# Kernel tuning notes

Hardware: AMD Instinct MI355X
Metric: run time of the kernel (lower is better)

## Reference

```python
import jax, jax.numpy as jnp
import numpy as np

LAYER = 2
B, L, N, N2, S, M, D = 128, 50, 12, 12, 20, 12, 100


def _l2norm(x, eps=1e-12):
    # torch F.normalize: x / max(||x||_2, eps) over last dim
    n = jnp.sqrt(jnp.sum(x * x, axis=-1, keepdims=True))
    return x / jnp.maximum(n, eps)


def setup_inputs() -> dict:
    key = jax.random.key(0)
    ks = jax.random.split(key, 10)
    return {
        "sess_self": jax.random.normal(ks[0], (B, L, D), jnp.float32),
        "sess_neighbor": jax.random.normal(ks[1], (B, L, N, D), jnp.float32),
        "sess_neighbor2": jax.random.normal(ks[2], (B, L, N, N2, D), jnp.float32),
        "tar_self": jax.random.normal(ks[3], (B, S, D), jnp.float32),
        "tar_neighbor": jax.random.normal(ks[4], (B, S, M, D), jnp.float32),
        "w1": jax.random.normal(ks[5], (LAYER, D, D), jnp.float32) * 0.1,
        "w2": jax.random.normal(ks[6], (LAYER, D, 1), jnp.float32) * 0.1,
        "w3": jax.random.normal(ks[7], (LAYER, 2 * D, D), jnp.float32) * 0.1,
        "w4": jax.random.normal(ks[8], (LAYER, D, 1), jnp.float32) * 0.1,
        "session_len": jax.random.randint(ks[9], (B,), 1, 50).astype(jnp.int64),
    }


def _forward(sess_self, sess_neighbor, sess_neighbor2, tar_self, tar_neighbor, w1, w2, w3, w4):
    b, s = sess_self.shape[0], tar_self.shape[1]
    l, d = sess_self.shape[1], sess_self.shape[2]
    # sess_embedding_layer: list of [B,S,L,D]; target: list of [B,S,D]
    sess_layers = [jnp.broadcast_to(sess_self[:, None, :, :], (b, s, l, d))]
    tar_layers = [tar_self]
    sn = sess_neighbor  # may be updated by 2-hop aggregation
    for i in range(LAYER):
        # --- session neighbor attention: mul -> linear -> leaky_relu -> linear -> softmax(N) -> sum ---
        mean_sess = jnp.mean(sess_layers[i], axis=1)                     # [B,L,D]
        att = (mean_sess[:, :, None, :] * sn) @ w1[i]                    # [B,L,N,D]
        att = jax.nn.leaky_relu(att, negative_slope=0.2)
        att = jax.nn.softmax(att @ w2[i], axis=-2)                       # [B,L,N,1]
        total = jnp.sum(att * sn, axis=-2)                               # [B,L,D]
        emb = _l2norm(total)
        sess_layers.append(jnp.broadcast_to(emb[:, None, :, :], (b, s, l, d)))
        # --- 2-hop neighbor aggregation (only first layer when layer>1) ---
        if i <= 0 and LAYER > 1:
            att2 = (sn[:, :, :, None, :] * sess_neighbor2) @ w1[i]       # [B,L,N,N2,D]
            att2 = jax.nn.leaky_relu(att2, negative_slope=0.2)
            att2 = jax.nn.softmax(att2 @ w2[i], axis=-2)                 # [B,L,N,N2,1]
            sn = jnp.sum(att2 * sess_neighbor2, axis=-2)                 # [B,L,N,D]
        # --- target neighbor attention ---
        sess_last = sess_layers[i - 1][:, :, :1, :]                      # [B,S,1,D]
        t = tar_layers[i]                                                # [B,S,D]
        cat = jnp.concatenate(
            [t[:, :, None, :] * tar_neighbor, sess_last + tar_neighbor], axis=-1)  # [B,S,M,2D]
        a = jnp.tanh(cat @ w3[i])                                        # [B,S,M,D]
        a = jax.nn.softmax(a @ w4[i], axis=-2)                           # [B,S,M,1]
        tot = jnp.sum(a * tar_neighbor, axis=-2)                         # [B,S,D]
        ti = _l2norm((tot + tar_layers[0]) * 0.5)
        tar_layers.append(ti)
        tar_layers = tar_layers + tar_layers  # faithful: list doubles each layer
    return jnp.stack(sess_layers, axis=0), jnp.stack(tar_layers, axis=0)


def reference(sess_self, sess_neighbor, sess_neighbor2, tar_self, tar_neighbor, w1, w2, w3, w4, session_len):
    return _forward(sess_self, sess_neighbor, sess_neighbor2, tar_self, tar_neighbor, w1, w2, w3, w4)
```

## Files before the change

kernel.cpp:

```cpp
#include <hip/hip_runtime.h>
#include <cmath>

#define CB 128
#define CL 50
#define CN 12
#define CS 20
#define CM 12
#define CD 100

typedef __attribute__((ext_vector_type(8))) short short8;
typedef __attribute__((ext_vector_type(4))) float f32x4;

__device__ __forceinline__ unsigned short f2bf(float f) {
    unsigned int u = __float_as_uint(f);
    u += 0x7FFFu + ((u >> 16) & 1u);
    return (unsigned short)(u >> 16);
}
__device__ __forceinline__ float4 mul4(float4 a, float4 b) {
    return make_float4(a.x * b.x, a.y * b.y, a.z * b.z, a.w * b.w);
}
__device__ __forceinline__ float4 add4(float4 a, float4 b) {
    return make_float4(a.x + b.x, a.y + b.y, a.z + b.z, a.w + b.w);
}
__device__ __forceinline__ short8 pack8(float4 a, float4 b) {
    short8 v;
    v[0] = (short)f2bf(a.x); v[1] = (short)f2bf(a.y);
    v[2] = (short)f2bf(a.z); v[3] = (short)f2bf(a.w);
    v[4] = (short)f2bf(b.x); v[5] = (short)f2bf(b.y);
    v[6] = (short)f2bf(b.z); v[7] = (short)f2bf(b.w);
    return v;
}

__global__ void prep_weights_kernel(const float* __restrict__ w1,
                                    const float* __restrict__ w3,
                                    unsigned short* __restrict__ w1t,
                                    unsigned short* __restrict__ w3t)
{
    int idx = blockIdx.x * 256 + threadIdx.x;
    const int TOT1 = 2 * 112 * 128;
    const int TOT3 = 2 * 112 * 224;
    if (idx < TOT1) {
        int l = idx / (112 * 128);
        int r = idx - l * (112 * 128);
        int n = r / 128, k = r - (r / 128) * 128;
        float v = (n < CD && k < CD) ? w1[l * CD * CD + k * CD + n] : 0.f;
        w1t[idx] = f2bf(v);
    } else if (idx < TOT1 + TOT3) {
        int j = idx - TOT1;
        int l = j / (112 * 224);
        int r = j - l * (112 * 224);
        int n = r / 224, k = r - (r / 224) * 224;
        float v = (n < CD && k < 2 * CD) ? w3[l * 2 * CD * CD + k * CD + n] : 0.f;
        w3t[j] = f2bf(v);
    }
}

__global__ __launch_bounds__(256) void neigh_mfma_kernel(
    const float* __restrict__ a0, const float* __restrict__ c0,
    float* __restrict__ o0, int nb0, int l20,
    const float* __restrict__ a1, const float* __restrict__ c1,
    float* __restrict__ o1, int l21,
    const unsigned short* __restrict__ w1t,
    const float* __restrict__ w2)
{
    __shared__ __align__(16) unsigned short sB[112 * 128];

    const int tid = threadIdx.x;
    const int wave = tid >> 6, lane = tid & 63;
    const int lhi = lane >> 4, llo = lane & 15;

    const float *ap, *cp; float* op; int l2f, g0;
    if ((int)blockIdx.x < nb0) {
        ap = a0; cp = c0; op = o0; l2f = l20; g0 = blockIdx.x * 4;
    } else {
        ap = a1; cp = c1; op = o1; l2f = l21; g0 = (blockIdx.x - nb0) * 4;
    }
    const int g = g0 + wave;

    for (int i = tid; i < 1792; i += 256) {
        int n = i >> 4, kc = i & 15;
        short8 v = *(const short8*)(w1t + n * 128 + kc * 8);
        char* dst = (char*)sB + n * 256 + ((kc ^ (n & 7)) << 4);
        *(short8*)dst = v;
    }

    short8 af[4];
    {
        const int n = (llo < CN) ? llo : 0;
        const float* cpr = cp + ((size_t)g * CN + n) * CD;
        const float* apr = ap + (size_t)g * CD;
#pragma unroll
        for (int ks = 0; ks < 4; ++ks) {
            const int k0 = ks * 32 + lhi * 8;
            if (ks < 3) {
                float4 cv0 = *(const float4*)(cpr + k0);
                float4 cv1 = *(const float4*)(cpr + k0 + 4);
                float4 av0 = *(const float4*)(apr + k0);
                float4 av1 = *(const float4*)(apr + k0 + 4);
                af[ks] = pack8(mul4(av0, cv0), mul4(av1, cv1));
            } else if (lhi == 0) {
                float4 cv0 = *(const float4*)(cpr + 96);
                float4 av0 = *(const float4*)(apr + 96);
                float4 z = make_float4(0.f, 0.f, 0.f, 0.f);
                af[ks] = pack8(mul4(av0, cv0), z);
            } else {
                af[ks] = (short8){0, 0, 0, 0, 0, 0, 0, 0};
            }
        }
    }
    __syncthreads();

    f32x4 acc[7];
#pragma unroll
    for (int nt = 0; nt < 7; ++nt) acc[nt] = (f32x4){0.f, 0.f, 0.f, 0.f};

    const char* pB = (const char*)sB;
    const int bxor = llo & 7;
#pragma unroll
    for (int ks = 0; ks < 4; ++ks) {
        const int kbq = ks * 4 + lhi;
#pragma unroll
        for (int nt = 0; nt < 7; ++nt) {
            short8 bfv = *(const short8*)(pB + (nt * 16 + llo) * 256 + ((kbq ^ bxor) << 4));
            acc[nt] = __builtin_amdgcn_mfma_f32_16x16x32_bf16(af[ks], bfv, acc[nt], 0, 0, 0);
        }
    }

    float s[4] = {0.f, 0.f, 0.f, 0.f};
#pragma unroll
    for (int nt = 0; nt < 7; ++nt) {
        const int n = nt * 16 + llo;
        const float w2v = (n < CD) ? w2[n] : 0.f;
#pragma unroll
        for (int r = 0; r < 4; ++r) {
            float y = acc[nt][r];
            y = (y >= 0.f) ? y : 0.2f * y;
            s[r] = fmaf(y, w2v, s[r]);
        }
    }
#pragma unroll
    for (int off = 1; off < 16; off <<= 1)
#pragma unroll
        for (int r = 0; r < 4; ++r) s[r] += __shfl_xor(s[r], off, 64);

    float pmax = -1e30f;
    if (lhi < 3) pmax = fmaxf(fmaxf(s[0], s[1]), fmaxf(s[2], s[3]));
    pmax = fmaxf(pmax, __shfl_xor(pmax, 16, 64));
    pmax = fmaxf(pmax, __shfl_xor(pmax, 32, 64));
    float e[4];
#pragma unroll
    for (int r = 0; r < 4; ++r) e[r] = (lhi < 3) ? __expf(s[r] - pmax) : 0.f;
    float ps = e[0] + e[1] + e[2] + e[3];
    ps += __shfl_xor(ps, 16, 64);
    ps += __shfl_xor(ps, 32, 64);
    const float inv = 1.f / ps;
    float att[4];
#pragma unroll
    for (int r = 0; r < 4; ++r) att[r] = e[r] * inv;

    float a12[12];
#pragma unroll
    for (int n = 0; n < 12; ++n)
        a12[n] = __shfl(att[n & 3], (n >> 2) * 16, 64);

    const bool act = lane < 50;
    const int d2 = lane * 2;
    float2 tot = make_float2(0.f, 0.f);
    if (act) {
        const float* crow = cp + (size_t)g * CN * CD + d2;
#pragma unroll
        for (int n = 0; n < CN; ++n) {
            float2 cv = *(const float2*)(crow + n * CD);
            tot.x = fmaf(a12[n], cv.x, tot.x);
            tot.y = fmaf(a12[n], cv.y, tot.y);
        }
    }
    if (l2f) {
        float sq = act ? (tot.x * tot.x + tot.y * tot.y) : 0.f;
#pragma unroll
        for (int off = 32; off > 0; off >>= 1) sq += __shfl_xor(sq, off, 64);
        const float rn = 1.f / fmaxf(sqrtf(sq), 1e-12f);
        tot.x *= rn; tot.y *= rn;
    }
    if (act) *(float2*)(op + (size_t)g * CD + d2) = tot;
}

__device__ __forceinline__ int swzq28(int q, int x) {
    return q ^ ((q < 24) ? x : (x & 3));
}
__device__ __forceinline__ float4 xchunk(const float* __restrict__ tnr,
                                         const float* __restrict__ tv,
                                         const float* __restrict__ slv, int k) {
    if (k < CD)
        return mul4(*(const float4*)(tv + k), *(const float4*)(tnr + k));
    if (k < 2 * CD) {
        int k2 = k - CD;
        return add4(*(const float4*)(slv + k2), *(const float4*)(tnr + k2));
    }
    return make_float4(0.f, 0.f, 0.f, 0.f);
}

__global__ __launch_bounds__(256, 3) void tar_mfma_kernel(
    const float* __restrict__ tvec,
    const float* __restrict__ sl,
    const float* __restrict__ tn,
    const unsigned short* __restrict__ w3t,
    const float* __restrict__ w4,
    const float* __restrict__ tar0,
    float* __restrict__ outp,
    int slStride)
{
    __shared__ __align__(16) unsigned short sB[112 * 224];
    __shared__ float s_score[128];
    __shared__ float s_att[96];
    __shared__ float s_sq[8][25];
    __shared__ float s_rn[8];

    const int tid = threadIdx.x;
    const int g0 = blockIdx.x * 8;
    const int wave = tid >> 6, lane = tid & 63;
    const int lhi = lane >> 4, llo = lane & 15;

    for (int i = tid; i < 3136; i += 256) {
        int n = i / 28, kc = i - (i / 28) * 28;
        short8 v = *(const short8*)(w3t + n * 224 + kc * 8);
        char* dst = (char*)sB + n * 448 + (swzq28(kc, n & 7) << 4);
        *(short8*)dst = v;
    }

    short8 af[2][7];
#pragma unroll
    for (int mt = 0; mt < 2; ++mt) {
        const int g = g0 + wave * 2 + mt;
        const int b = g / CS;
        const int m = (llo < CM) ? llo : 0;
        const float* tnr = tn + ((size_t)g * CM + m) * CD;
        const float* tv = tvec + (size_t)g * CD;
        const float* slv = sl + (size_t)b * slStride;
#pragma unroll
        for (int ks = 0; ks < 7; ++ks) {
            const int k0 = ks * 32 + lhi * 8;
            af[mt][ks] = pack8(xchunk(tnr, tv, slv, k0),
                               xchunk(tnr, tv, slv, k0 + 4));
        }
    }
    __syncthreads();

    f32x4 acc[2][7];
#pragma unroll
    for (int mt = 0; mt < 2; ++mt)
#pragma unroll
        for (int nt = 0; nt < 7; ++nt)
            acc[mt][nt] = (f32x4){0.f, 0.f, 0.f, 0.f};

    const char* pB = (const char*)sB;
    const int bxor = llo & 7;
#pragma unroll
    for (int ks = 0; ks < 7; ++ks) {
        const int kbq = ks * 4 + lhi;
        short8 bf[7];
#pragma unroll
        for (int nt = 0; nt < 7; ++nt)
            bf[nt] = *(const short8*)(pB + (nt * 16 + llo) * 448 + (swzq28(kbq, bxor) << 4));
#pragma unroll
        for (int mt = 0; mt < 2; ++mt)
#pragma unroll
            for (int nt = 0; nt < 7; ++nt)
                acc[mt][nt] = __builtin_amdgcn_mfma_f32_16x16x32_bf16(
                    af[mt][ks], bf[nt], acc[mt][nt], 0, 0, 0);
    }

    float w4v[7];
#pragma unroll
    for (int nt = 0; nt < 7; ++nt) {
        int n = nt * 16 + llo;
        w4v[nt] = (n < CD) ? w4[n] : 0.f;
    }
#pragma unroll
    for (int mt = 0; mt < 2; ++mt) {
        float s[4] = {0.f, 0.f, 0.f, 0.f};
#pragma unroll
        for (int nt = 0; nt < 7; ++nt)
#pragma unroll
            for (int r = 0; r < 4; ++r)
                s[r] = fmaf(tanhf(acc[mt][nt][r]), w4v[nt], s[r]);
#pragma unroll
        for (int off = 1; off < 16; off <<= 1)
#pragma unroll
            for (int r = 0; r < 4; ++r) s[r] += __shfl_xor(s[r], off, 64);
        if (llo == 0) {
            int rowb = wave * 32 + mt * 16 + lhi * 4;
#pragma unroll
            for (int r = 0; r < 4; ++r) s_score[rowb + r] = s[r];
        }
    }
    __syncthreads();

    if (tid < 96) {
        const int g = tid / 12;
        const int m = tid - g * 12;
        const float* sr = s_score + g * 16;
        float mx = -1e30f;
#pragma unroll
        for (int j = 0; j < CM; ++j) mx = fmaxf(mx, sr[j]);
        float sum = 0.f;
#pragma unroll
        for (int j = 0; j < CM; ++j) sum += __expf(sr[j] - mx);
        s_att[tid] = __expf(sr[m] - mx) / sum;
    }
    __syncthreads();

    const bool act = tid < 200;
    int gl = tid / 25, d4 = tid % 25;
    float4 tot = make_float4(0.f, 0.f, 0.f, 0.f);
    if (act) {
        const float* tnr = tn + (size_t)(g0 + gl) * CM * CD + d4 * 4;
#pragma unroll
        for (int m = 0; m < CM; ++m) {
            float4 cv = *(const float4*)(tnr + m * CD);
            float at = s_att[gl * CM + m];
            tot.x = fmaf(at, cv.x, tot.x);
            tot.y = fmaf(at, cv.y, tot.y);
            tot.z = fmaf(at, cv.z, tot.z);
            tot.w = fmaf(at, cv.w, tot.w);
        }
        float4 t0 = *(const float4*)(tar0 + (size_t)(g0 + gl) * CD + d4 * 4);
        tot.x = (tot.x + t0.x) * 0.5f;
        tot.y = (tot.y + t0.y) * 0.5f;
        tot.z = (tot.z + t0.z) * 0.5f;
        tot.w = (tot.w + t0.w) * 0.5f;
        s_sq[gl][d4] = tot.x * tot.x + tot.y * tot.y + tot.z * tot.z + tot.w * tot.w;
    }
    __syncthreads();
    if (tid < 8) {
        float sq = 0.f;
        for (int j = 0; j < 25; ++j) sq += s_sq[tid][j];
        s_rn[tid] = 1.f / fmaxf(sqrtf(sq), 1e-12f);
    }
    __syncthreads();
    if (act) {
        float rn = s_rn[gl];
        tot.x *= rn; tot.y *= rn; tot.z *= rn;
        tot.w *= rn;
        *(float4*)(outp + (size_t)(g0 + gl) * CD + d4 * 4) = tot;
    }
}

__global__ void assemble_kernel(
    const float* __restrict__ sess_self, const float* __restrict__ emb0,
    const float* __restrict__ emb1, const float* __restrict__ tar_self,
    const float* __restrict__ T1, const float* __restrict__ T2,
    float4* __restrict__ out)
{
    const int LD4 = CL * CD / 4;
    const int SLD4 = CS * LD4;
    const int LAY0 = CB * SLD4;
    const int TOT0 = 3 * LAY0;
    const int LAY1 = CB * CS * CD / 4;
    const int TOT = TOT0 + 10 * LAY1;

    for (int i = blockIdx.x * blockDim.x + threadIdx.x; i < TOT;
         i += gridDim.x * blockDim.x) {
        float4 v;
        if (i < TOT0) {
            int layer = i / LAY0;
            int r = i - layer * LAY0;
            int b = r / SLD4;
            int r2 = r - b * SLD4;
            int ld4 = r2 % LD4;
            const float* src = (layer == 0) ? sess_self : (layer == 1) ? emb0 : emb1;
            v = ((const float4*)src)[b * LD4 + ld4];
        } else {
            int j = i - TOT0;
            int layer = j / LAY1;
            int r = j - layer * LAY1;
            int k = layer % 5;
            const float* src = (k == 4) ? T2 : ((k == 1) || (k == 3)) ? T1 : tar_self;
            v = ((const float4*)src)[r];
        }
        out[i] = v;
    }
}

extern "C" void kernel_launch(void* const* d_in, const int* in_sizes, int n_in,
                              void* d_out, int out_size, void* d_ws, size_t ws_size,
                              hipStream_t stream)
{
    const float* sess_self      = (const float*)d_in[0];
    const float* sess_neighbor  = (const float*)d_in[1];
    const float* sess_neighbor2 = (const float*)d_in[2];
    const float* tar_self       = (const float*)d_in[3];
    const float* tar_neighbor   = (const float*)d_in[4];
    const float* w1             = (const float*)d_in[5];
    const float* w2             = (const float*)d_in[6];
    const float* w3             = (const float*)d_in[7];
    const float* w4             = (const float*)d_in[8];
    float* out = (float*)d_out;
    float* ws  = (float*)d_ws;

    float* emb0 = ws;
    float* emb1 = ws + 640000;
    float* sn1  = ws + 1280000;
    float* T1   = ws + 8960000;
    float* T2   = ws + 9216000;
    unsigned short* w1t = (unsigned short*)(ws + 9472000);
    unsigned short* w3t = w1t + 28672;

    prep_weights_kernel<<<308, 256, 0, stream>>>(w1, w3, w1t, w3t);

    neigh_mfma_kernel<<<20800, 256, 0, stream>>>(
        sess_self, sess_neighbor, emb0, 1600, 1,
        sess_neighbor, sess_neighbor2, sn1, 0,
        w1t, w2);
    neigh_mfma_kernel<<<1600, 256, 0, stream>>>(
        emb0, sn1, emb1, 1600, 1,
        emb0, sn1, emb1, 1,
        w1t + 112 * 128, w2 + CD);
    tar_mfma_kernel<<<320, 256, 0, stream>>>(
        tar_self, emb0, tar_neighbor, w3t, w4, tar_self, T1, CL * CD);
    tar_mfma_kernel<<<320, 256, 0, stream>>>(
        T1, sess_self, tar_neighbor, w3t + 112 * 224, w4 + CD, tar_self, T2, CL * CD);

    assemble_kernel<<<2048, 256, 0, stream>>>(
        sess_self, emb0, emb1, tar_self, T1, T2, (float4*)out);
}
```

Measured before the change: 292.9 us.

## Rebalance rows per wave in neighbor and target MFMA kernels; nontemporal output stores

The neighbor attention kernel now has each wave handle two row groups instead of one. Each shared-memory B fragment is reused across two MFMAs, and half as many blocks reload the W1 tile into LDS. The target kernel goes the other way: one group per wave with in-register softmax and norm via shuffles, dropping the shared-memory score buffers and extra block barriers, and it launches twice the blocks without the occupancy hint. The assemble kernel switches to nontemporal stores for the large output write. The trade-offs are higher register pressure in the neighbor kernel and more redundant W3 staging in the target kernel.

```diff
diff --git a/kernel.cpp b/kernel.cpp
--- a/kernel.cpp
+++ b/kernel.cpp
@@ -71,11 +71,10 @@
 
     const float *ap, *cp; float* op; int l2f, g0;
     if ((int)blockIdx.x < nb0) {
-        ap = a0; cp = c0; op = o0; l2f = l20; g0 = blockIdx.x * 4;
+        ap = a0; cp = c0; op = o0; l2f = l20; g0 = blockIdx.x * 8;
     } else {
-        ap = a1; cp = c1; op = o1; l2f = l21; g0 = (blockIdx.x - nb0) * 4;
-    }
-    const int g = g0 + wave;
+        ap = a1; cp = c1; op = o1; l2f = l21; g0 = (blockIdx.x - nb0) * 8;
+    }
 
     for (int i = tid; i < 1792; i += 256) {
         int n = i >> 4, kc = i & 15;
@@ -84,8 +83,10 @@
         *(short8*)dst = v;
     }
 
-    short8 af[4];
-    {
+    short8 af[2][4];
+#pragma unroll
+    for (int mt = 0; mt < 2; ++mt) {
+        const int g = g0 + wave * 2 + mt;
         const int n = (llo < CN) ? llo : 0;
         const float* cpr = cp + ((size_t)g * CN + n) * CD;
         const float* apr = ap + (size_t)g * CD;
@@ -97,22 +98,24 @@
                 float4 cv1 = *(const float4*)(cpr + k0 + 4);
                 float4 av0 = *(const float4*)(apr + k0);
                 float4 av1 = *(const float4*)(apr + k0 + 4);
-                af[ks] = pack8(mul4(av0, cv0), mul4(av1, cv1));
+                af[mt][ks] = pack8(mul4(av0, cv0), mul4(av1, cv1));
             } else if (lhi == 0) {
                 float4 cv0 = *(const float4*)(cpr + 96);
                 float4 av0 = *(const float4*)(apr + 96);
                 float4 z = make_float4(0.f, 0.f, 0.f, 0.f);
-                af[ks] = pack8(mul4(av0, cv0), z);
+                af[mt][ks] = pack8(mul4(av0, cv0), z);
             } else {
-                af[ks] = (short8){0, 0, 0, 0, 0, 0, 0, 0};
+                af[mt][ks] = (short8){0, 0, 0, 0, 0, 0, 0, 0};
             }
         }
     }
     __syncthreads();
 
-    f32x4 acc[7];
-#pragma unroll
-    for (int nt = 0; nt < 7; ++nt) acc[nt] = (f32x4){0.f, 0.f, 0.f, 0.f};
+    f32x4 acc[2][7];
+#pragma unroll
+    for (int mt = 0; mt < 2; ++mt)
+#pragma unroll
+        for (int nt = 0; nt < 7; ++nt) acc[mt][nt] = (f32x4){0.f, 0.f, 0.f, 0.f};
 
     const char* pB = (const char*)sB;
     const int bxor = llo & 7;
@@ -122,67 +125,70 @@
 #pragma unroll
         for (int nt = 0; nt < 7; ++nt) {
             short8 bfv = *(const short8*)(pB + (nt * 16 + llo) * 256 + ((kbq ^ bxor) << 4));
-            acc[nt] = __builtin_amdgcn_mfma_f32_16x16x32_bf16(af[ks], bfv, acc[nt], 0, 0, 0);
-        }
-    }
-
-    float s[4] = {0.f, 0.f, 0.f, 0.f};
-#pragma unroll
-    for (int nt = 0; nt < 7; ++nt) {
-        const int n = nt * 16 + llo;
-        const float w2v = (n < CD) ? w2[n] : 0.f;
-#pragma unroll
-        for (int r = 0; r < 4; ++r) {
-            float y = acc[nt][r];
-            y = (y >= 0.f) ? y : 0.2f * y;
-            s[r] = fmaf(y, w2v, s[r]);
-        }
-    }
-#pragma unroll
-    for (int off = 1; off < 16; off <<= 1)
-#pragma unroll
-        for (int r = 0; r < 4; ++r) s[r] += __shfl_xor(s[r], off, 64);
-
-    float pmax = -1e30f;
-    if (lhi < 3) pmax = fmaxf(fmaxf(s[0], s[1]), fmaxf(s[2], s[3]));
-    pmax = fmaxf(pmax, __shfl_xor(pmax, 16, 64));
-    pmax = fmaxf(pmax, __shfl_xor(pmax, 32, 64));
-    float e[4];
-#pragma unroll
-    for (int r = 0; r < 4; ++r) e[r] = (lhi < 3) ? __expf(s[r] - pmax) : 0.f;
-    float ps = e[0] + e[1] + e[2] + e[3];
-    ps += __shfl_xor(ps, 16, 64);
-    ps += __shfl_xor(ps, 32, 64);
-    const float inv = 1.f / ps;
-    float att[4];
-#pragma unroll
-    for (int r = 0; r < 4; ++r) att[r] = e[r] * inv;
-
-    float a12[12];
-#pragma unroll
-    for (int n = 0; n < 12; ++n)
-        a12[n] = __shfl(att[n & 3], (n >> 2) * 16, 64);
+            acc[0][nt] = __builtin_amdgcn_mfma_f32_16x16x32_bf16(af[0][ks], bfv, acc[0][nt], 0, 0, 0);
+            acc[1][nt] = __builtin_amdgcn_mfma_f32_16x16x32_bf16(af[1][ks], bfv, acc[1][nt], 0, 0, 0);
+        }
+    }
+
+    float att[2][4];
+#pragma unroll
+    for (int mt = 0; mt < 2; ++mt) {
+        float s[4] = {0.f, 0.f, 0.f, 0.f};
+#pragma unroll
+        for (int nt = 0; nt < 7; ++nt) {
+            const int n = nt * 16 + llo;
+            const float w2v = (n < CD) ? w2[n] : 0.f;
+#pragma unroll
+            for (int r = 0; r < 4; ++r) {
+                float y = acc[mt][nt][r];
+                y = (y >= 0.f) ? y : 0.2f * y;
+                s[r] = fmaf(y, w2v, s[r]);
+            }
+        }
+#pragma unroll
+        for (int off = 1; off < 16; off <<= 1)
+#pragma unroll
+            for (int r = 0; r < 4; ++r) s[r] += __shfl_xor(s[r], off, 64);
+        float pmax = -1e30f;
+        if (lhi < 3) pmax = fmaxf(fmaxf(s[0], s[1]), fmaxf(s[2], s[3]));
+        pmax = fmaxf(pmax, __shfl_xor(pmax, 16, 64));
+        pmax = fmaxf(pmax, __shfl_xor(pmax, 32, 64));
+        float e[4];
+#pragma unroll
+        for (int r = 0; r < 4; ++r) e[r] = (lhi < 3) ? __expf(s[r] - pmax) : 0.f;
+        float ps = e[0] + e[1] + e[2] + e[3];
+        ps += __shfl_xor(ps, 16, 64);
+        ps += __shfl_xor(ps, 32, 64);
+        const float inv = 1.f / ps;
+#pragma unroll
+        for (int r = 0; r < 4; ++r) att[mt][r] = e[r] * inv;
+    }
 
     const bool act = lane < 50;
     const int d2 = lane * 2;
-    float2 tot = make_float2(0.f, 0.f);
-    if (act) {
-        const float* crow = cp + (size_t)g * CN * CD + d2;
-#pragma unroll
-        for (int n = 0; n < CN; ++n) {
-            float2 cv = *(const float2*)(crow + n * CD);
-            tot.x = fmaf(a12[n], cv.x, tot.x);
-            tot.y = fmaf(a12[n], cv.y, tot.y);
-        }
-    }
-    if (l2f) {
-        float sq = act ? (tot.x * tot.x + tot.y * tot.y) : 0.f;
-#pragma unroll
-        for (int off = 32; off > 0; off >>= 1) sq += __shfl_xor(sq, off, 64);
-        const float rn = 1.f / fmaxf(sqrtf(sq), 1e-12f);
-        tot.x *= rn; tot.y *= rn;
-    }
-    if (act) *(float2*)(op + (size_t)g * CD + d2) = tot;
+#pragma unroll
+    for (int mt = 0; mt < 2; ++mt) {
+        const int g = g0 + wave * 2 + mt;
+        float2 tot = make_float2(0.f, 0.f);
+        if (act) {
+            const float* crow = cp + (size_t)g * CN * CD + d2;
+#pragma unroll
+            for (int n = 0; n < CN; ++n) {
+                const float at = __shfl(att[mt][n & 3], (n >> 2) * 16, 64);
+                float2 cv = *(const float2*)(crow + n * CD);
+                tot.x = fmaf(at, cv.x, tot.x);
+                tot.y = fmaf(at, cv.y, tot.y);
+            }
+        }
+        if (l2f) {
+            float sq = act ? (tot.x * tot.x + tot.y * tot.y) : 0.f;
+#pragma unroll
+            for (int off = 32; off > 0; off >>= 1) sq += __shfl_xor(sq, off, 64);
+            const float rn = 1.f / fmaxf(sqrtf(sq), 1e-12f);
+            tot.x *= rn; tot.y *= rn;
+        }
+        if (act) *(float2*)(op + (size_t)g * CD + d2) = tot;
+    }
 }
 
 __device__ __forceinline__ int swzq28(int q, int x) {
@@ -200,7 +206,7 @@
     return make_float4(0.f, 0.f, 0.f, 0.f);
 }
 
-__global__ __launch_bounds__(256, 3) void tar_mfma_kernel(
+__global__ __launch_bounds__(256) void tar_mfma_kernel(
     const float* __restrict__ tvec,
     const float* __restrict__ sl,
     const float* __restrict__ tn,
@@ -211,15 +217,12 @@
     int slStride)
 {
     __shared__ __align__(16) unsigned short sB[112 * 224];
-    __shared__ float s_score[128];
-    __shared__ float s_att[96];
-    __shared__ float s_sq[8][25];
-    __shared__ float s_rn[8];
 
     const int tid = threadIdx.x;
-    const int g0 = blockIdx.x * 8;
     const int wave = tid >> 6, lane = tid & 63;
     const int lhi = lane >> 4, llo = lane & 15;
+    const int g = blockIdx.x * 4 + wave;
+    const int b = g / CS;
 
     for (int i = tid; i < 3136; i += 256) {
         int n = i / 28, kc = i - (i / 28) * 28;
@@ -228,11 +231,8 @@
         *(short8*)dst = v;
     }
 
-    short8 af[2][7];
-#pragma unroll
-    for (int mt = 0; mt < 2; ++mt) {
-        const int g = g0 + wave * 2 + mt;
-        const int b = g / CS;
+    short8 af[7];
+    {
         const int m = (llo < CM) ? llo : 0;
         const float* tnr = tn + ((size_t)g * CM + m) * CD;
         const float* tv = tvec + (size_t)g * CD;
@@ -240,109 +240,80 @@
 #pragma unroll
         for (int ks = 0; ks < 7; ++ks) {
             const int k0 = ks * 32 + lhi * 8;
-            af[mt][ks] = pack8(xchunk(tnr, tv, slv, k0),
-                               xchunk(tnr, tv, slv, k0 + 4));
+            af[ks] = pack8(xchunk(tnr, tv, slv, k0),
+                           xchunk(tnr, tv, slv, k0 + 4));
         }
     }
     __syncthreads();
 
-    f32x4 acc[2][7];
-#pragma unroll
-    for (int mt = 0; mt < 2; ++mt)
-#pragma unroll
-        for (int nt = 0; nt < 7; ++nt)
-            acc[mt][nt] = (f32x4){0.f, 0.f, 0.f, 0.f};
+    f32x4 acc[7];
+#pragma unroll
+    for (int nt = 0; nt < 7; ++nt) acc[nt] = (f32x4){0.f, 0.f, 0.f, 0.f};
 
     const char* pB = (const char*)sB;
     const int bxor = llo & 7;
 #pragma unroll
     for (int ks = 0; ks < 7; ++ks) {
         const int kbq = ks * 4 + lhi;
-        short8 bf[7];
-#pragma unroll
-        for (int nt = 0; nt < 7; ++nt)
-            bf[nt] = *(const short8*)(pB + (nt * 16 + llo) * 448 + (swzq28(kbq, bxor) << 4));
-#pragma unroll
-        for (int mt = 0; mt < 2; ++mt)
-#pragma unroll
-            for (int nt = 0; nt < 7; ++nt)
-                acc[mt][nt] = __builtin_amdgcn_mfma_f32_16x16x32_bf16(
-                    af[mt][ks], bf[nt], acc[mt][nt], 0, 0, 0);
-    }
-
-    float w4v[7];
+#pragma unroll
+        for (int nt = 0; nt < 7; ++nt) {
+            short8 bfv = *(const short8*)(pB + (nt * 16 + llo) * 448 + (swzq28(kbq, bxor) << 4));
+            acc[nt] = __builtin_amdgcn_mfma_f32_16x16x32_bf16(af[ks], bfv, acc[nt], 0, 0, 0);
+        }
+    }
+
+    float s[4] = {0.f, 0.f, 0.f, 0.f};
 #pragma unroll
     for (int nt = 0; nt < 7; ++nt) {
-        int n = nt * 16 + llo;
-        w4v[nt] = (n < CD) ? w4[n] : 0.f;
-    }
-#pragma unroll
-    for (int mt = 0; mt < 2; ++mt) {
-        float s[4] = {0.f, 0.f, 0.f, 0.f};
-#pragma unroll
-        for (int nt = 0; nt < 7; ++nt)
-#pragma unroll
-            for (int r = 0; r < 4; ++r)
-                s[r] = fmaf(tanhf(acc[mt][nt][r]), w4v[nt], s[r]);
-#pragma unroll
-        for (int off = 1; off < 16; off <<= 1)
-#pragma unroll
-            for (int r = 0; r < 4; ++r) s[r] += __shfl_xor(s[r], off, 64);
-        if (llo == 0) {
-            int rowb = wave * 32 + mt * 16 + lhi * 4;
-#pragma unroll
-            for (int r = 0; r < 4; ++r) s_score[rowb + r] = s[r];
-        }
-    }
-    __syncthreads();
-
-    if (tid < 96) {
-        const int g = tid / 12;
-        const int m = tid - g * 12;
-        const float* sr = s_score + g * 16;
-        float mx = -1e30f;
-#pragma unroll
-        for (int j = 0; j < CM; ++j) mx = fmaxf(mx, sr[j]);
-        float sum = 0.f;
-#pragma unroll
-        for (int j = 0; j < CM; ++j) sum += __expf(sr[j] - mx);
-        s_att[tid] = __expf(sr[m] - mx) / sum;
-    }
-    __syncthreads();
-
-    const bool act = tid < 200;
-    int gl = tid / 25, d4 = tid % 25;
-    float4 tot = make_float4(0.f, 0.f, 0.f, 0.f);
+        const int n = nt * 16 + llo;
+        const float w4v = (n < CD) ? w4[n] : 0.f;
+#pragma unroll
+        for (int r = 0; r < 4; ++r)
+            s[r] = fmaf(tanhf(acc[nt][r]), w4v, s[r]);
+    }
+#pragma unroll
+    for (int off = 1; off < 16; off <<= 1)
+#pragma unroll
+        for (int r = 0; r < 4; ++r) s[r] += __shfl_xor(s[r], off, 64);
+
+    float pmax = -1e30f;
+    if (lhi < 3) pmax = fmaxf(fmaxf(s[0], s[1]), fmaxf(s[2], s[3]));
+    pmax = fmaxf(pmax, __shfl_xor(pmax, 16, 64));
+    pmax = fmaxf(pmax, __shfl_xor(pmax, 32, 64));
+    float e[4];
+#pragma unroll
+    for (int r = 0; r < 4; ++r) e[r] = (lhi < 3) ? __expf(s[r] - pmax) : 0.f;
+    float ps = e[0] + e[1] + e[2] + e[3];
+    ps += __shfl_xor(ps, 16, 64);
+    ps += __shfl_xor(ps, 32, 64);
+    const float inv = 1.f / ps;
+    float att[4];
+#pragma unroll
+    for (int r = 0; r < 4; ++r) att[r] = e[r] * inv;
+
+    const bool act = lane < 50;
+    const int d2 = lane * 2;
+    float2 tot = make_float2(0.f, 0.f);
     if (act) {
-        const float* tnr = tn + (size_t)(g0 + gl) * CM * CD + d4 * 4;
+        const float* tnr = tn + (size_t)g * CM * CD + d2;
 #pragma unroll
         for (int m = 0; m < CM; ++m) {
-            float4 cv = *(const float4*)(tnr + m * CD);
-            float at = s_att[gl * CM + m];
+            const float at = __shfl(att[m & 3], (m >> 2) * 16, 64);
+            float2 cv = *(const float2*)(tnr + m * CD);
             tot.x = fmaf(at, cv.x, tot.x);
             tot.y = fmaf(at, cv.y, tot.y);
-            tot.z = fmaf(at, cv.z, tot.z);
-            tot.w = fmaf(at, cv.w, tot.w);
-        }
-        float4 t0 = *(const float4*)(tar0 + (size_t)(g0 + gl) * CD + d4 * 4);
+        }
+        float2 t0 = *(const float2*)(tar0 + (size_t)g * CD + d2);
         tot.x = (tot.x + t0.x) * 0.5f;
         tot.y = (tot.y + t0.y) * 0.5f;
-        tot.z = (tot.z + t0.z) * 0.5f;
-        tot.w = (tot.w + t0.w) * 0.5f;
-        s_sq[gl][d4] = tot.x * tot.x + tot.y * tot.y + tot.z * tot.z + tot.w * tot.w;
-    }
-    __syncthreads();
-    if (tid < 8) {
-        float sq = 0.f;
-        for (int j = 0; j < 25; ++j) sq += s_sq[tid][j];
-        s_rn[tid] = 1.f / fmaxf(sqrtf(sq), 1e-12f);
-    }
-    __syncthreads();
+    }
+    float sq = act ? (tot.x * tot.x + tot.y * tot.y) : 0.f;
+#pragma unroll
+    for (int off = 32; off > 0; off >>= 1) sq += __shfl_xor(sq, off, 64);
+    const float rn = 1.f / fmaxf(sqrtf(sq), 1e-12f);
     if (act) {
-        float rn = s_rn[gl];
-        tot.x *= rn; tot.y *= rn; tot.z *= rn;
-        tot.w *= rn;
-        *(float4*)(outp + (size_t)(g0 + gl) * CD + d4 * 4) = tot;
+        tot.x *= rn; tot.y *= rn;
+        *(float2*)(outp + (size_t)g * CD + d2) = tot;
     }
 }
 
@@ -350,7 +321,7 @@
     const float* __restrict__ sess_self, const float* __restrict__ emb0,
     const float* __restrict__ emb1, const float* __restrict__ tar_self,
     const float* __restrict__ T1, const float* __restrict__ T2,
-    float4* __restrict__ out)
+    f32x4* __restrict__ out)
 {
     const int LD4 = CL * CD / 4;
     const int SLD4 = CS * LD4;
@@ -361,7 +332,7 @@
 
     for (int i = blockIdx.x * blockDim.x + threadIdx.x; i < TOT;
          i += gridDim.x * blockDim.x) {
-        float4 v;
+        f32x4 v;
         if (i < TOT0) {
             int layer = i / LAY0;
             int r = i - layer * LAY0;
@@ -369,16 +340,16 @@
             int r2 = r - b * SLD4;
             int ld4 = r2 % LD4;
             const float* src = (layer == 0) ? sess_self : (layer == 1) ? emb0 : emb1;
-            v = ((const float4*)src)[b * LD4 + ld4];
+            v = ((const f32x4*)src)[b * LD4 + ld4];
         } else {
             int j = i - TOT0;
             int layer = j / LAY1;
             int r = j - layer * LAY1;
             int k = layer % 5;
             const float* src = (k == 4) ? T2 : ((k == 1) || (k == 3)) ? T1 : tar_self;
-            v = ((const float4*)src)[r];
-        }
-        out[i] = v;
+            v = ((const f32x4*)src)[r];
+        }
+        __builtin_nontemporal_store(v, &out[i]);
     }
 }
 
@@ -408,19 +379,19 @@
 
     prep_weights_kernel<<<308, 256, 0, stream>>>(w1, w3, w1t, w3t);
 
-    neigh_mfma_kernel<<<20800, 256, 0, stream>>>(
-        sess_self, sess_neighbor, emb0, 1600, 1,
+    neigh_mfma_kernel<<<10400, 256, 0, stream>>>(
+        sess_self, sess_neighbor, emb0, 800, 1,
         sess_neighbor, sess_neighbor2, sn1, 0,
         w1t, w2);
-    neigh_mfma_kernel<<<1600, 256, 0, stream>>>(
-        emb0, sn1, emb1, 1600, 1,
+    neigh_mfma_kernel<<<800, 256, 0, stream>>>(
+        emb0, sn1, emb1, 800, 1,
         emb0, sn1, emb1, 1,
         w1t + 112 * 128, w2 + CD);
-    tar_mfma_kernel<<<320, 256, 0, stream>>>(
+    tar_mfma_kernel<<<640, 256, 0, stream>>>(
         tar_self, emb0, tar_neighbor, w3t, w4, tar_self, T1, CL * CD);
-    tar_mfma_kernel<<<320, 256, 0, stream>>>(
+    tar_mfma_kernel<<<640, 256, 0, stream>>>(
         T1, sess_self, tar_neighbor, w3t + 112 * 224, w4 + CD, tar_self, T2, CL * CD);
 
     assemble_kernel<<<2048, 256, 0, stream>>>(
-        sess_self, emb0, emb1, tar_self, T1, T2, (float4*)out);
-}
+        sess_self, emb0, emb1, tar_self, T1, T2, (f32x4*)out);
+}
```

After: 279.7 us. 4.5% less time.
